# Kernel tuning notes

Hardware: AMD Instinct MI355X
Metric: run time of the kernel (lower is better)

The kernel has to match this reference:

```python
import jax, jax.numpy as jnp
import numpy as np

BIG = 1e6  # z-buffer sentinel for 'no hit'
EPS = 1e-8


def batch_orth_proj(X, camera):
    # X: [B,N,3], camera: [B,3] = (scale, tx, ty)  (DECA util.batch_orth_proj)
    cam = camera.reshape(-1, 1, 3)
    xy = X[..., :2] + cam[..., 1:]
    Xt = jnp.concatenate([xy, X[..., 2:]], axis=-1)
    return cam[..., 0:1] * Xt


def transform_verts(verts, cam):
    t = batch_orth_proj(verts, cam)
    # t[...,1:] = -t[...,1:]; t[...,2] += 10; clamp xy to [-1,1]
    x = jnp.clip(t[..., 0:1], -1.0, 1.0)
    y = jnp.clip(-t[..., 1:2], -1.0, 1.0)
    z = -t[..., 2:3] + 10.0
    return jnp.concatenate([x, y, z], axis=-1)


def face_vertices(vertices, faces):
    # vertices [B,N,C], faces [F,3] -> [B,F,3,C]
    return vertices[:, faces]


def rasterize(verts, faces, attrs, H, W, chunk=512):
    # verts [B,N,3] in NDC ([-1,1] xy, z depth), faces [F,3] int, attrs [B,F,3,C]
    B, N, _ = verts.shape
    F = faces.shape[0]
    C = attrs.shape[-1]
    P = H * W
    ii, jj = jnp.meshgrid(jnp.arange(H), jnp.arange(W), indexing='ij')
    px = ((jj.reshape(-1).astype(verts.dtype) + 0.5) / W * 2.0 - 1.0)  # [P]
    py = ((ii.reshape(-1).astype(verts.dtype) + 0.5) / H * 2.0 - 1.0)
    n_chunks = F // chunk
    faces_c = faces.reshape(n_chunks, chunk, 3)
    attrs_c = attrs.reshape(B, n_chunks, chunk, 3, C).transpose(1, 0, 2, 3, 4)
    b_idx = jnp.arange(B)[:, None]
    p_idx = jnp.arange(P)[None, :]

    def step(carry, inp):
        best_z, best_attr, alpha = carry
        f, a = inp  # f [chunk,3], a [B,chunk,3,C]
        fv = verts[:, f]                      # [B,chunk,3,3]
        v0, v1, v2 = fv[:, :, 0], fv[:, :, 1], fv[:, :, 2]
        # edge vectors, broadcast shapes: pixel [1,P,1], face [B,1,chunk]
        e1x = (v1[..., 0] - v0[..., 0])[:, None]
        e1y = (v1[..., 1] - v0[..., 1])[:, None]
        e2x = (v2[..., 0] - v0[..., 0])[:, None]
        e2y = (v2[..., 1] - v0[..., 1])[:, None]
        d = e1x * e2y - e2x * e1y             # [B,1,chunk]
        inv = 1.0 / jnp.where(jnp.abs(d) > EPS, d, 1.0)
        dpx = px[None, :, None] - v0[..., 0][:, None]
        dpy = py[None, :, None] - v0[..., 1][:, None]
        w1 = (dpx * e2y - e2x * dpy) * inv    # [B,P,chunk]
        w2 = (e1x * dpy - dpx * e1y) * inv
        w0 = 1.0 - w1 - w2
        inside = (w0 >= 0) & (w1 >= 0) & (w2 >= 0) & (jnp.abs(d) > EPS)
        z = (w0 * v0[..., 2][:, None] + w1 * v1[..., 2][:, None]
             + w2 * v2[..., 2][:, None])
        z = jnp.where(inside, z, BIG)
        idx = jnp.argmin(z, axis=-1)          # [B,P] winning face in chunk
        zb = z[b_idx, p_idx, idx]
        w0b = w0[b_idx, p_idx, idx]
        w1b = w1[b_idx, p_idx, idx]
        w2b = w2[b_idx, p_idx, idx]
        af = a[b_idx, idx]                    # [B,P,3,C]
        pix = (w0b[..., None] * af[:, :, 0] + w1b[..., None] * af[:, :, 1]
               + w2b[..., None] * af[:, :, 2])
        upd = zb < best_z
        best_z = jnp.where(upd, zb, best_z)
        best_attr = jnp.where(upd[..., None], pix, best_attr)
        alpha = jnp.where(zb < BIG * 0.5, 1.0, alpha)
        return (best_z, best_attr, alpha), None

    init = (jnp.full((B, P), BIG, verts.dtype),
            jnp.zeros((B, P, C), verts.dtype),
            jnp.zeros((B, P), verts.dtype))
    (bz, ba, al), _ = jax.lax.scan(step, init, (faces_c, attrs_c))
    out = jnp.concatenate([ba, al[..., None]], axis=-1)  # [B,P,C+1]
    return out.reshape(B, H, W, C + 1).transpose(0, 3, 1, 2)


def grid_sample(img, grid):
    # img [B,C,H,W], grid [B,Hg,Wg,2] in [-1,1]; bilinear, zeros pad, align_corners=False
    B, C, H, W = img.shape
    x = (grid[..., 0] + 1.0) * 0.5 * W - 0.5
    y = (grid[..., 1] + 1.0) * 0.5 * H - 0.5
    x0 = jnp.floor(x); y0 = jnp.floor(y)
    wx1 = x - x0; wx0 = 1.0 - wx1
    wy1 = y - y0; wy0 = 1.0 - wy1
    b = jnp.arange(B)[:, None, None]

    def fetch(ix, iy):
        valid = (ix >= 0) & (ix < W) & (iy >= 0) & (iy < H)
        ixc = jnp.clip(ix, 0, W - 1).astype(jnp.int32)
        iyc = jnp.clip(iy, 0, H - 1).astype(jnp.int32)
        v = img[b, :, iyc, ixc]               # [B,Hg,Wg,C]
        return v * valid[..., None]

    out = (wy0[..., None] * (wx0[..., None] * fetch(x0, y0) + wx1[..., None] * fetch(x0 + 1, y0))
           + wy1[..., None] * (wx0[..., None] * fetch(x0, y0 + 1) + wx1[..., None] * fetch(x0 + 1, y0 + 1)))
    return out.transpose(0, 3, 1, 2)          # [B,C,Hg,Wg]


def setup_inputs() -> dict:
    key = jax.random.key(0)
    k1, k2, k3, k4, k5 = jax.random.split(key, 5)
    B, N, F, H, W = 2, 5120, 10240, 256, 256
    return {
        'cam': jax.random.uniform(k1, (B, 3), jnp.float32),
        'head_vertices': jax.random.normal(k2, (B, N, 3), jnp.float32),
        'images': jax.random.uniform(k3, (B, 3, H, W), jnp.float32),
        'cam_new': jax.random.uniform(k4, (B, 3), jnp.float32),
        'faces': jax.random.randint(k5, (F, 3), 0, N, dtype=jnp.int32),
    }


def reference(cam, head_vertices, images, cam_new, faces):
    H = W = images.shape[-1]
    # UV path (old camera): uvcoords = [clamped xy, 1], per-face attrs (detached)
    t_verts = transform_verts(head_vertices, cam)
    uvcoords = jnp.concatenate(
        [t_verts[..., :2], jnp.ones_like(t_verts[..., :1])], axis=-1)
    attributes = jax.lax.stop_gradient(face_vertices(uvcoords, faces))  # [B,F,3,3]
    # Geometry path (new camera)
    transformed = transform_verts(head_vertices, cam_new)
    rendering = rasterize(transformed, faces, attributes, H, W)  # [B,4,H,W]
    grid = rendering[:, :3].transpose(0, 2, 3, 1)[..., :2]      # [B,H,W,2]
    results = grid_sample(images, grid)
    return results
```

## Files before the change

### kernel.cpp

```cpp
#include <hip/hip_runtime.h>
#include <stdint.h>

typedef unsigned int uint;
typedef unsigned long long ull;


#define K_BUCKETS 4096
#define ZLO 0.0f
#define ZHI 20.0f
#define TOL 2.5e-4f
#define NSEG 64
#define PAD 0.004f
#define GROUP 4

__device__ __forceinline__ float clip11(float t) {
  return fminf(1.0f, fmaxf(-1.0f, t));
}

__device__ __forceinline__ float RL(float v, int j) {
  return __uint_as_float((uint)__builtin_amdgcn_readlane((int)__float_as_uint(v), j));
}

__global__ void k_faces(const int* __restrict__ faces,
                        const float* __restrict__ hv,
                        const float* __restrict__ cam,
                        const float* __restrict__ camn,
                        float4* __restrict__ fh4,
                        float4* __restrict__ fa4,
                        uint* __restrict__ bkt,
                        uint* __restrict__ cnt,
                        ull* __restrict__ packed, int np,
                        int F, int N, int B) {
#pragma clang fp contract(off)
  int t = blockIdx.x * 256 + threadIdx.x;
  int nthr = gridDim.x * 256;
  for (int i = t; i < np; i += nthr) packed[i] = 0xFFFFFFFFFFFFFFFFull;
  if (t >= B * F) return;
  int b = t / F;
  int f = t - b * F;
  int i0 = faces[f * 3 + 0];
  int i1 = faces[f * 3 + 1];
  int i2 = faces[f * 3 + 2];
  float c0n = camn[b * 3 + 0], c1n = camn[b * 3 + 1], c2n = camn[b * 3 + 2];
  float c0o = cam[b * 3 + 0], c1o = cam[b * 3 + 1], c2o = cam[b * 3 + 2];

  float x0, y0, z0, x1, y1, z1, x2, y2, z2;
  float u0, v0, u1, v1, u2, v2;
#define XFORM(idx, X, Y, Z, U, V)                          \
  {                                                        \
    const float* p = hv + (size_t)(b * N + (idx)) * 3;     \
    float X0 = p[0], X1 = p[1], X2 = p[2];                 \
    float t0 = c0n * (X0 + c1n);                           \
    float t1 = c0n * (X1 + c2n);                           \
    float t2 = c0n * X2;                                   \
    X = clip11(t0);                                        \
    Y = clip11(-t1);                                       \
    Z = -t2 + 10.0f;                                       \
    float s0 = c0o * (X0 + c1o);                           \
    float s1 = c0o * (X1 + c2o);                           \
    U = clip11(s0);                                        \
    V = clip11(-s1);                                       \
  }
  XFORM(i0, x0, y0, z0, u0, v0)
  XFORM(i1, x1, y1, z1, u1, v1)
  XFORM(i2, x2, y2, z2, u2, v2)
#undef XFORM

  float e1x = x1 - x0;
  float e1y = y1 - y0;
  float e2x = x2 - x0;
  float e2y = y2 - y0;
  float d = (e1x * e2y) - (e2x * e1y);
  float inv;
  if (fabsf(d) > 1e-8f) {
    inv = 1.0f / d;
  } else {
    inv = __int_as_float(0x7fc00000);
  }
  float4* fq = fh4 + (size_t)t * 4;
  fq[0] = make_float4(fminf(x0, fminf(x1, x2)), fmaxf(x0, fmaxf(x1, x2)),
                      fminf(y0, fminf(y1, y2)), fmaxf(y0, fmaxf(y1, y2)));
  fq[1] = make_float4(x0, y0, e1x, e1y);
  fq[2] = make_float4(e2x, e2y, inv, z0);
  fq[3] = make_float4(z1, z2, 0.0f, 0.0f);

  float zmn = fminf(z0, fminf(z1, z2));
  int kb = (int)((zmn - ZLO) * ((float)K_BUCKETS / (ZHI - ZLO)));
  kb = min(max(kb, 0), K_BUCKETS - 1);
  bkt[t] = (uint)kb;
  atomicAdd(&cnt[b * K_BUCKETS + kb], 1u);

  float4* aq = fa4 + (size_t)t * 2;
  aq[0] = make_float4(u0, v0, u1, v1);
  aq[1] = make_float4(u2, v2, 0.0f, 0.0f);
}

__global__ void __launch_bounds__(1024) k_prefix(const uint* __restrict__ cnt,
                                                 uint* __restrict__ off) {
  __shared__ uint s[1024];
  int b = blockIdx.x;
  const uint* c = cnt + (size_t)b * K_BUCKETS;
  uint* o = off + (size_t)b * K_BUCKETS;
  int tid = threadIdx.x;
  uint v0 = c[tid * 4 + 0], v1 = c[tid * 4 + 1], v2 = c[tid * 4 + 2], v3 = c[tid * 4 + 3];
  uint sum = v0 + v1 + v2 + v3;
  s[tid] = sum;
  __syncthreads();
  for (int d = 1; d < 1024; d <<= 1) {
    uint t = (tid >= d) ? s[tid - d] : 0u;
    __syncthreads();
    s[tid] += t;
    __syncthreads();
  }
  uint run = s[tid] - sum;
  o[tid * 4 + 0] = run; run += v0;
  o[tid * 4 + 1] = run; run += v1;
  o[tid * 4 + 2] = run; run += v2;
  o[tid * 4 + 3] = run;
}

__global__ void k_scatter(const float4* __restrict__ fh4,
                          const uint* __restrict__ bkt,
                          uint* __restrict__ off,
                          float4* __restrict__ s3,
                          float4* __restrict__ bboxs,
                          float* __restrict__ lbC,
                          int F, int NCH64, int B) {
  int t = blockIdx.x * 256 + threadIdx.x;
  if (t >= B * F) return;
  int b = t / F;
  int f = t - b * F;
  uint kb = bkt[t];
  uint pos = atomicAdd(&off[b * K_BUCKETS + kb], 1u);
  const float4* s = fh4 + (size_t)t * 4;
  float4 q0 = s[0], q1 = s[1], q2 = s[2], q3 = s[3];
  q3.z = __uint_as_float((uint)f);
  q3.w = (kb == 0u) ? -1e30f : (ZLO + (float)kb * ((ZHI - ZLO) / (float)K_BUCKETS));
  float4* d = s3 + ((size_t)b * F + pos) * 3;
  d[0] = q1; d[1] = q2; d[2] = q3;
  bboxs[(size_t)b * F + pos] = q0;
  if ((pos & 63u) == 0u) lbC[b * NCH64 + (pos >> 6)] = q3.w;
}

__global__ void __launch_bounds__(128) k_raster(const float4* __restrict__ s3,
                                                const float4* __restrict__ bboxs,
                                                const float* __restrict__ lbC,
                                                ull* __restrict__ packed,
                                                int F, int NCH64, int B) {
#pragma clang fp contract(off)
  int w = blockIdx.x * 2 + (threadIdx.x >> 6);
  int lane = threadIdx.x & 63;
  int tilesPerSeg = B * 1024;
  int s = w / tilesPerSeg;
  int rem = w - s * tilesPerSeg;
  int b = rem >> 10;
  int tile = rem & 1023;
  int tx = tile & 31, ty = tile >> 5;
  int col = tx * 8 + (lane & 7);
  int row = ty * 8 + (lane >> 3);

  float px = (col + 0.5f) / 256.0f * 2.0f - 1.0f;
  float py = (row + 0.5f) / 256.0f * 2.0f - 1.0f;
  float txlo = (tx * 8 + 0.5f) / 256.0f * 2.0f - 1.0f - PAD;
  float txhi = (tx * 8 + 7.5f) / 256.0f * 2.0f - 1.0f + PAD;
  float tylo = (ty * 8 + 0.5f) / 256.0f * 2.0f - 1.0f - PAD;
  float tyhi = (ty * 8 + 7.5f) / 256.0f * 2.0f - 1.0f + PAD;

  const float4* __restrict__ s3B = s3 + (size_t)b * F * 3;
  const float4* __restrict__ bbB = bboxs + (size_t)b * F;
  const float* __restrict__ lbB = lbC + b * NCH64;
  size_t pix = ((size_t)b << 16) + (row << 8) + col;

  ull best = 0xFFFFFFFFFFFFFFFFull, pub = 0xFFFFFFFFFFFFFFFFull;

  int cps = (NCH64 + NSEG - 1) / NSEG;
  int ch0 = s * cps;
  int ch1 = min(NCH64, ch0 + cps);
  if (ch0 >= ch1) return;

  float4 bbCur = bbB[(size_t)(ch0 * 64 + lane)];

  for (int cg = ch0; cg < ch1; cg += GROUP) {
    ull pk = __hip_atomic_load(packed + pix, __ATOMIC_RELAXED,
                               __HIP_MEMORY_SCOPE_AGENT);
    float kz = fminf(__uint_as_float((uint)(best >> 32)),
                     __uint_as_float((uint)(pk >> 32)));
    float lb = lbB[cg];
    if (__all(lb >= kz + TOL)) break;

    int cend = min(cg + GROUP, ch1);
    for (int ch = cg; ch < cend; ++ch) {
      int ni = (ch + 1 < ch1) ? ch + 1 : ch;
      float4 bbNxt = bbB[(size_t)(ni * 64 + lane)];

      int si = ch * 64 + lane;
      bool ok = (bbCur.x <= txhi && bbCur.y >= txlo &&
                 bbCur.z <= tyhi && bbCur.w >= tylo);
      float4 r1 = bbCur, r2 = bbCur, r3 = bbCur;
      if (ok) {
        r1 = s3B[(size_t)si * 3 + 0];
        r2 = s3B[(size_t)si * 3 + 1];
        float ax = r1.x, ay = r1.y;
        float e1x = r1.z, e1y = r1.w;
        float e2x = r2.x, e2y = r2.y;
        float sg = r2.z;
        float e3x = e2x - e1x, e3y = e2y - e1y;
        float bxx = ax + e1x, bxy = ay + e1y;
        float nx = -sg * e1y, ny = sg * e1x;
        float dotA = nx * ((nx > 0.0f ? txhi : txlo) - ax) +
                     ny * ((ny > 0.0f ? tyhi : tylo) - ay);
        nx = sg * e2y; ny = -sg * e2x;
        float dotB = nx * ((nx > 0.0f ? txhi : txlo) - ax) +
                     ny * ((ny > 0.0f ? tyhi : tylo) - ay);
        nx = -sg * e3y; ny = sg * e3x;
        float dotC = nx * ((nx > 0.0f ? txhi : txlo) - bxx) +
                     ny * ((ny > 0.0f ? tyhi : tylo) - bxy);
        ok = !(dotA < 0.0f) && !(dotB < 0.0f) && !(dotC < 0.0f);
      }
      if (ok) r3 = s3B[(size_t)si * 3 + 2];

      ull m = __ballot(ok);
      while (m) {
        int j = (int)__builtin_ctzll(m);
        m &= m - 1;
        float v0x = RL(r1.x, j), v0y = RL(r1.y, j);
        float e1x = RL(r1.z, j), e1y = RL(r1.w, j);
        float e2x = RL(r2.x, j), e2y = RL(r2.y, j);
        float inv = RL(r2.z, j), z0 = RL(r2.w, j);
        float z1 = RL(r3.x, j), z2 = RL(r3.y, j);
        uint fo = (uint)__builtin_amdgcn_readlane((int)__float_as_uint(r3.z), j);
        float dpx = px - v0x;
        float dpy = py - v0y;
        float w1 = (dpx * e2y - e2x * dpy) * inv;
        float w2 = (e1x * dpy - dpx * e1y) * inv;
        float w0 = (1.0f - w1) - w2;
        bool inside = (w0 >= 0.0f) && (w1 >= 0.0f) && (w2 >= 0.0f);
        float z = (w0 * z0 + w1 * z1) + w2 * z2;
        ull cand = ((ull)__float_as_uint(z) << 32) | (ull)fo;
        best = (inside && cand < best) ? cand : best;
      }
      bbCur = bbNxt;
    }
    if (best < pub) { atomicMin(packed + pix, best); pub = best; }
  }
  if (best < pub) atomicMin(packed + pix, best);
}

__device__ __forceinline__ float fetchpix(const float* __restrict__ img, int base,
                                          float ixf, float iyf) {
  bool valid = (ixf >= 0.0f) && (ixf < 256.0f) && (iyf >= 0.0f) && (iyf < 256.0f);
  int ix = (int)fminf(255.0f, fmaxf(0.0f, ixf));
  int iy = (int)fminf(255.0f, fmaxf(0.0f, iyf));
  float v = img[base + iy * 256 + ix];
  return valid ? v : 0.0f;
}

__global__ void __launch_bounds__(256) k_sample(const float4* __restrict__ fh4,
                                                const float4* __restrict__ fa4,
                                                const ull* __restrict__ packed,
                                                const float* __restrict__ img,
                                                float* __restrict__ out,
                                                int F) {
#pragma clang fp contract(off)
  int t = blockIdx.x * 256 + threadIdx.x;
  int b = t >> 16;
  int pix = t & 65535;
  int row = pix >> 8;
  int col = pix & 255;
  float px = (col + 0.5f) / 256.0f * 2.0f - 1.0f;
  float py = (row + 0.5f) / 256.0f * 2.0f - 1.0f;

  ull pk = packed[t];
  uint f = (uint)pk;
  float gx = 0.0f, gy = 0.0f;
  if (f != 0xFFFFFFFFu) {
    const float4* fq = fh4 + ((size_t)b * F + f) * 4;
    float4 q1 = fq[1];
    float4 q2 = fq[2];
    float dpx = px - q1.x;
    float dpy = py - q1.y;
    float w1 = (dpx * q2.y - q2.x * dpy) * q2.z;
    float w2 = (q1.z * dpy - dpx * q1.w) * q2.z;
    float w0 = (1.0f - w1) - w2;
    const float4* aq = fa4 + ((size_t)b * F + f) * 2;
    float4 a0 = aq[0];
    float4 a1 = aq[1];
    gx = (w0 * a0.x + w1 * a0.z) + w2 * a1.x;
    gy = (w0 * a0.y + w1 * a0.w) + w2 * a1.y;
  }

  float x = (gx + 1.0f) * 0.5f * 256.0f - 0.5f;
  float y = (gy + 1.0f) * 0.5f * 256.0f - 0.5f;
  float x0f = floorf(x), y0f = floorf(y);
  float wx1 = x - x0f, wx0 = 1.0f - wx1;
  float wy1 = y - y0f, wy0 = 1.0f - wy1;

  for (int ch = 0; ch < 3; ++ch) {
    int base = (b * 3 + ch) * 65536;
    float f00 = fetchpix(img, base, x0f, y0f);
    float f10 = fetchpix(img, base, x0f + 1.0f, y0f);
    float f01 = fetchpix(img, base, x0f, y0f + 1.0f);
    float f11 = fetchpix(img, base, x0f + 1.0f, y0f + 1.0f);
    float A  = wy0 * ((wx0 * f00) + (wx1 * f10));
    float Bv = wy1 * ((wx0 * f01) + (wx1 * f11));
    out[base + pix] = A + Bv;
  }
}

extern "C" void kernel_launch(void* const* d_in, const int* in_sizes, int n_in,
                              void* d_out, int out_size, void* d_ws, size_t ws_size,
                              hipStream_t stream) {
  const float* cam  = (const float*)d_in[0];
  const float* hv   = (const float*)d_in[1];
  const float* img  = (const float*)d_in[2];
  const float* camn = (const float*)d_in[3];
  const int* faces  = (const int*)d_in[4];

  const int B = in_sizes[0] / 3;
  const int N = in_sizes[1] / (3 * B);
  const int F = in_sizes[4] / 3;
  const int NCH64 = (F + 63) / 64;
  const int P = 65536;

  char* wsb = (char*)d_ws;
  size_t ofs = 0;
  float4* fh4   = (float4*)(wsb + ofs); ofs += (size_t)B * F * 4 * sizeof(float4);
  float4* fa4   = (float4*)(wsb + ofs); ofs += (size_t)B * F * 2 * sizeof(float4);
  float4* s3    = (float4*)(wsb + ofs); ofs += (size_t)B * F * 3 * sizeof(float4);
  float4* bboxs = (float4*)(wsb + ofs); ofs += (size_t)B * F * sizeof(float4);
  uint* bkt = (uint*)(wsb + ofs); ofs += (size_t)B * F * 4;
  uint* cnt = (uint*)(wsb + ofs); ofs += (size_t)B * K_BUCKETS * 4;
  uint* off = (uint*)(wsb + ofs); ofs += (size_t)B * K_BUCKETS * 4;
  float* lbC = (float*)(wsb + ofs); ofs += (size_t)B * NCH64 * 4;
  ofs = (ofs + 255) & ~(size_t)255;
  ull* packed = (ull*)(wsb + ofs); ofs += (size_t)B * P * sizeof(ull);

  int np = B * P;
  hipMemsetAsync(cnt, 0, (size_t)B * K_BUCKETS * 4, stream);
  int nf = B * F;
  k_faces<<<(nf + 255) / 256, 256, 0, stream>>>(faces, hv, cam, camn,
                                                fh4, fa4, bkt, cnt,
                                                packed, np, F, N, B);
  k_prefix<<<B, 1024, 0, stream>>>(cnt, off);
  k_scatter<<<(nf + 255) / 256, 256, 0, stream>>>(fh4, bkt, off, s3, bboxs,
                                                  lbC, F, NCH64, B);
  const int cps = (NCH64 + NSEG - 1) / NSEG;
  const int segUsed = (NCH64 + cps - 1) / cps;
  int nwaves = segUsed * B * 1024;
  k_raster<<<nwaves / 2, 128, 0, stream>>>(s3, bboxs, lbC, packed, F, NCH64, B);
  k_sample<<<(np + 255) / 256, 256, 0, stream>>>(fh4, fa4, packed, img, (float*)d_out, F);
}
```

Measured before the change: 86.53 us.

## Fuse face prep, prefix scan and scatter into one cooperative kernel

Replaces the memset plus three separate launches (face transform and bucket count, prefix scan, scatter) with a single cooperative kernel that uses grid-wide syncs between phases. The count buffer is now zeroed inside the kernel, and the prefix scan runs in 256-thread blocks with 16 elements per thread. The aim is to remove per-launch overhead and inter-kernel gaps on the small preprocessing stages, at the cost of grid.sync barriers and the requirement that all 80 blocks be co-resident.

New measurement: 122.6 us. +41.6%, slower.

```diff
diff --git a/kernel.cpp b/kernel.cpp
--- a/kernel.cpp
+++ b/kernel.cpp
@@ -1,5 +1,8 @@
 #include <hip/hip_runtime.h>
+#include <hip/hip_cooperative_groups.h>
 #include <stdint.h>
+
+namespace cg = cooperative_groups;
 
 typedef unsigned int uint;
 typedef unsigned long long ull;
@@ -21,125 +24,131 @@
   return __uint_as_float((uint)__builtin_amdgcn_readlane((int)__float_as_uint(v), j));
 }
 
-__global__ void k_faces(const int* __restrict__ faces,
-                        const float* __restrict__ hv,
-                        const float* __restrict__ cam,
-                        const float* __restrict__ camn,
-                        float4* __restrict__ fh4,
-                        float4* __restrict__ fa4,
-                        uint* __restrict__ bkt,
-                        uint* __restrict__ cnt,
-                        ull* __restrict__ packed, int np,
-                        int F, int N, int B) {
+__global__ void __launch_bounds__(256) k_prep(const int* __restrict__ faces,
+                                              const float* __restrict__ hv,
+                                              const float* __restrict__ cam,
+                                              const float* __restrict__ camn,
+                                              float4* __restrict__ fh4,
+                                              float4* __restrict__ fa4,
+                                              uint* __restrict__ bkt,
+                                              uint* __restrict__ cnt,
+                                              uint* __restrict__ off,
+                                              float4* __restrict__ s3,
+                                              float4* __restrict__ bboxs,
+                                              float* __restrict__ lbC,
+                                              ull* __restrict__ packed,
+                                              int np, int F, int N, int B,
+                                              int NCH64) {
 #pragma clang fp contract(off)
+  cg::grid_group grid = cg::this_grid();
   int t = blockIdx.x * 256 + threadIdx.x;
   int nthr = gridDim.x * 256;
+  int BF = B * F;
+  int ncnt = B * K_BUCKETS;
+
   for (int i = t; i < np; i += nthr) packed[i] = 0xFFFFFFFFFFFFFFFFull;
-  if (t >= B * F) return;
-  int b = t / F;
-  int f = t - b * F;
-  int i0 = faces[f * 3 + 0];
-  int i1 = faces[f * 3 + 1];
-  int i2 = faces[f * 3 + 2];
-  float c0n = camn[b * 3 + 0], c1n = camn[b * 3 + 1], c2n = camn[b * 3 + 2];
-  float c0o = cam[b * 3 + 0], c1o = cam[b * 3 + 1], c2o = cam[b * 3 + 2];
-
-  float x0, y0, z0, x1, y1, z1, x2, y2, z2;
-  float u0, v0, u1, v1, u2, v2;
+  for (int i = t; i < ncnt; i += nthr) cnt[i] = 0u;
+  grid.sync();
+
+  if (t < BF) {
+    int b = t / F;
+    int f = t - b * F;
+    int i0 = faces[f * 3 + 0];
+    int i1 = faces[f * 3 + 1];
+    int i2 = faces[f * 3 + 2];
+    float c0n = camn[b * 3 + 0], c1n = camn[b * 3 + 1], c2n = camn[b * 3 + 2];
+    float c0o = cam[b * 3 + 0], c1o = cam[b * 3 + 1], c2o = cam[b * 3 + 2];
+
+    float x0, y0, z0, x1, y1, z1, x2, y2, z2;
+    float u0, v0, u1, v1, u2, v2;
 #define XFORM(idx, X, Y, Z, U, V)                          \
-  {                                                        \
-    const float* p = hv + (size_t)(b * N + (idx)) * 3;     \
-    float X0 = p[0], X1 = p[1], X2 = p[2];                 \
-    float t0 = c0n * (X0 + c1n);                           \
-    float t1 = c0n * (X1 + c2n);                           \
-    float t2 = c0n * X2;                                   \
-    X = clip11(t0);                                        \
-    Y = clip11(-t1);                                       \
-    Z = -t2 + 10.0f;                                       \
-    float s0 = c0o * (X0 + c1o);                           \
-    float s1 = c0o * (X1 + c2o);                           \
-    U = clip11(s0);                                        \
-    V = clip11(-s1);                                       \
-  }
-  XFORM(i0, x0, y0, z0, u0, v0)
-  XFORM(i1, x1, y1, z1, u1, v1)
-  XFORM(i2, x2, y2, z2, u2, v2)
+    {                                                      \
+      const float* p = hv + (size_t)(b * N + (idx)) * 3;   \
+      float X0 = p[0], X1 = p[1], X2 = p[2];               \
+      float t0 = c0n * (X0 + c1n);                         \
+      float t1 = c0n * (X1 + c2n);                         \
+      float t2 = c0n * X2;                                 \
+      X = clip11(t0);                                      \
+      Y = clip11(-t1);                                     \
+      Z = -t2 + 10.0f;                                     \
+      float s0 = c0o * (X0 + c1o);                         \
+      float s1 = c0o * (X1 + c2o);                         \
+      U = clip11(s0);                                      \
+      V = clip11(-s1);                                     \
+    }
+    XFORM(i0, x0, y0, z0, u0, v0)
+    XFORM(i1, x1, y1, z1, u1, v1)
+    XFORM(i2, x2, y2, z2, u2, v2)
 #undef XFORM
 
-  float e1x = x1 - x0;
-  float e1y = y1 - y0;
-  float e2x = x2 - x0;
-  float e2y = y2 - y0;
-  float d = (e1x * e2y) - (e2x * e1y);
-  float inv;
-  if (fabsf(d) > 1e-8f) {
-    inv = 1.0f / d;
-  } else {
-    inv = __int_as_float(0x7fc00000);
-  }
-  float4* fq = fh4 + (size_t)t * 4;
-  fq[0] = make_float4(fminf(x0, fminf(x1, x2)), fmaxf(x0, fmaxf(x1, x2)),
-                      fminf(y0, fminf(y1, y2)), fmaxf(y0, fmaxf(y1, y2)));
-  fq[1] = make_float4(x0, y0, e1x, e1y);
-  fq[2] = make_float4(e2x, e2y, inv, z0);
-  fq[3] = make_float4(z1, z2, 0.0f, 0.0f);
-
-  float zmn = fminf(z0, fminf(z1, z2));
-  int kb = (int)((zmn - ZLO) * ((float)K_BUCKETS / (ZHI - ZLO)));
-  kb = min(max(kb, 0), K_BUCKETS - 1);
-  bkt[t] = (uint)kb;
-  atomicAdd(&cnt[b * K_BUCKETS + kb], 1u);
-
-  float4* aq = fa4 + (size_t)t * 2;
-  aq[0] = make_float4(u0, v0, u1, v1);
-  aq[1] = make_float4(u2, v2, 0.0f, 0.0f);
-}
-
-__global__ void __launch_bounds__(1024) k_prefix(const uint* __restrict__ cnt,
-                                                 uint* __restrict__ off) {
-  __shared__ uint s[1024];
-  int b = blockIdx.x;
-  const uint* c = cnt + (size_t)b * K_BUCKETS;
-  uint* o = off + (size_t)b * K_BUCKETS;
-  int tid = threadIdx.x;
-  uint v0 = c[tid * 4 + 0], v1 = c[tid * 4 + 1], v2 = c[tid * 4 + 2], v3 = c[tid * 4 + 3];
-  uint sum = v0 + v1 + v2 + v3;
-  s[tid] = sum;
-  __syncthreads();
-  for (int d = 1; d < 1024; d <<= 1) {
-    uint t = (tid >= d) ? s[tid - d] : 0u;
+    float e1x = x1 - x0;
+    float e1y = y1 - y0;
+    float e2x = x2 - x0;
+    float e2y = y2 - y0;
+    float d = (e1x * e2y) - (e2x * e1y);
+    float inv;
+    if (fabsf(d) > 1e-8f) {
+      inv = 1.0f / d;
+    } else {
+      inv = __int_as_float(0x7fc00000);
+    }
+    float4* fq = fh4 + (size_t)t * 4;
+    fq[0] = make_float4(fminf(x0, fminf(x1, x2)), fmaxf(x0, fmaxf(x1, x2)),
+                        fminf(y0, fminf(y1, y2)), fmaxf(y0, fmaxf(y1, y2)));
+    fq[1] = make_float4(x0, y0, e1x, e1y);
+    fq[2] = make_float4(e2x, e2y, inv, z0);
+    fq[3] = make_float4(z1, z2, 0.0f, 0.0f);
+
+    float zmn = fminf(z0, fminf(z1, z2));
+    int kb = (int)((zmn - ZLO) * ((float)K_BUCKETS / (ZHI - ZLO)));
+    kb = min(max(kb, 0), K_BUCKETS - 1);
+    bkt[t] = (uint)kb;
+    atomicAdd(&cnt[b * K_BUCKETS + kb], 1u);
+
+    float4* aq = fa4 + (size_t)t * 2;
+    aq[0] = make_float4(u0, v0, u1, v1);
+    aq[1] = make_float4(u2, v2, 0.0f, 0.0f);
+  }
+  grid.sync();
+
+  __shared__ uint s[256];
+  if ((int)blockIdx.x < B) {
+    int b = blockIdx.x;
+    const uint* c = cnt + (size_t)b * K_BUCKETS;
+    uint* o = off + (size_t)b * K_BUCKETS;
+    int tid = threadIdx.x;
+    uint v[16];
+    uint sum = 0;
+#pragma unroll
+    for (int k = 0; k < 16; ++k) { v[k] = c[tid * 16 + k]; sum += v[k]; }
+    s[tid] = sum;
     __syncthreads();
-    s[tid] += t;
-    __syncthreads();
-  }
-  uint run = s[tid] - sum;
-  o[tid * 4 + 0] = run; run += v0;
-  o[tid * 4 + 1] = run; run += v1;
-  o[tid * 4 + 2] = run; run += v2;
-  o[tid * 4 + 3] = run;
-}
-
-__global__ void k_scatter(const float4* __restrict__ fh4,
-                          const uint* __restrict__ bkt,
-                          uint* __restrict__ off,
-                          float4* __restrict__ s3,
-                          float4* __restrict__ bboxs,
-                          float* __restrict__ lbC,
-                          int F, int NCH64, int B) {
-  int t = blockIdx.x * 256 + threadIdx.x;
-  if (t >= B * F) return;
-  int b = t / F;
-  int f = t - b * F;
-  uint kb = bkt[t];
-  uint pos = atomicAdd(&off[b * K_BUCKETS + kb], 1u);
-  const float4* s = fh4 + (size_t)t * 4;
-  float4 q0 = s[0], q1 = s[1], q2 = s[2], q3 = s[3];
-  q3.z = __uint_as_float((uint)f);
-  q3.w = (kb == 0u) ? -1e30f : (ZLO + (float)kb * ((ZHI - ZLO) / (float)K_BUCKETS));
-  float4* d = s3 + ((size_t)b * F + pos) * 3;
-  d[0] = q1; d[1] = q2; d[2] = q3;
-  bboxs[(size_t)b * F + pos] = q0;
-  if ((pos & 63u) == 0u) lbC[b * NCH64 + (pos >> 6)] = q3.w;
+    for (int dd = 1; dd < 256; dd <<= 1) {
+      uint tt = (tid >= dd) ? s[tid - dd] : 0u;
+      __syncthreads();
+      s[tid] += tt;
+      __syncthreads();
+    }
+    uint run = s[tid] - sum;
+#pragma unroll
+    for (int k = 0; k < 16; ++k) { o[tid * 16 + k] = run; run += v[k]; }
+  }
+  grid.sync();
+
+  if (t < BF) {
+    int b = t / F;
+    int f = t - b * F;
+    uint kb = bkt[t];
+    uint pos = atomicAdd(&off[b * K_BUCKETS + kb], 1u);
+    const float4* sp = fh4 + (size_t)t * 4;
+    float4 q0 = sp[0], q1 = sp[1], q2 = sp[2], q3 = sp[3];
+    q3.z = __uint_as_float((uint)f);
+    q3.w = (kb == 0u) ? -1e30f : (ZLO + (float)kb * ((ZHI - ZLO) / (float)K_BUCKETS));
+    float4* d = s3 + ((size_t)b * F + pos) * 3;
+    d[0] = q1; d[1] = q2; d[2] = q3;
+    bboxs[(size_t)b * F + pos] = q0;
+    if ((pos & 63u) == 0u) lbC[b * NCH64 + (pos >> 6)] = q3.w;
+  }
 }
 
 __global__ void __launch_bounds__(128) k_raster(const float4* __restrict__ s3,
@@ -310,11 +319,11 @@
 extern "C" void kernel_launch(void* const* d_in, const int* in_sizes, int n_in,
                               void* d_out, int out_size, void* d_ws, size_t ws_size,
                               hipStream_t stream) {
+  const int* faces  = (const int*)d_in[4];
   const float* cam  = (const float*)d_in[0];
   const float* hv   = (const float*)d_in[1];
   const float* img  = (const float*)d_in[2];
   const float* camn = (const float*)d_in[3];
-  const int* faces  = (const int*)d_in[4];
 
   const int B = in_sizes[0] / 3;
   const int N = in_sizes[1] / (3 * B);
@@ -336,14 +345,19 @@
   ull* packed = (ull*)(wsb + ofs); ofs += (size_t)B * P * sizeof(ull);
 
   int np = B * P;
-  hipMemsetAsync(cnt, 0, (size_t)B * K_BUCKETS * 4, stream);
   int nf = B * F;
-  k_faces<<<(nf + 255) / 256, 256, 0, stream>>>(faces, hv, cam, camn,
-                                                fh4, fa4, bkt, cnt,
-                                                packed, np, F, N, B);
-  k_prefix<<<B, 1024, 0, stream>>>(cnt, off);
-  k_scatter<<<(nf + 255) / 256, 256, 0, stream>>>(fh4, bkt, off, s3, bboxs,
-                                                  lbC, F, NCH64, B);
+  int nblk = (nf + 255) / 256;
+
+  {
+    void* args[] = {(void*)&faces, (void*)&hv, (void*)&cam, (void*)&camn,
+                    (void*)&fh4, (void*)&fa4, (void*)&bkt, (void*)&cnt,
+                    (void*)&off, (void*)&s3, (void*)&bboxs, (void*)&lbC,
+                    (void*)&packed, (void*)&np, (void*)&F, (void*)&N,
+                    (void*)&B, (void*)&NCH64};
+    hipLaunchCooperativeKernel((const void*)k_prep, dim3(nblk), dim3(256),
+                               args, 0, stream);
+  }
+
   const int cps = (NCH64 + NSEG - 1) / NSEG;
   const int segUsed = (NCH64 + cps - 1) / cps;
   int nwaves = segUsed * B * 1024;
```
